# Performance work log

Measured on AMD Instinct MI355X. Metric: run time of the kernel, lower is better.

Reference implementation:

```python
import jax, jax.numpy as jnp
import numpy as np
from jax import lax

WINDOW_SIZE = 11
SIGMA = 1.5
DATA_RANGE = 1.0


def gaussian_window(size, sigma):
    k = jnp.arange(size, dtype=jnp.float32) - size // 2
    k = jnp.exp(-0.5 / sigma ** 2 * k ** 2)
    return k / k.sum()


def depthwise_conv(x, window):
    # x: [B,C,H,W], window: [C,1,k,k]
    pad = WINDOW_SIZE // 2
    return lax.conv_general_dilated(
        x, window,
        window_strides=(1, 1),
        padding=[(pad, pad), (pad, pad)],
        dimension_numbers=('NCHW', 'OIHW', 'NCHW'),
        feature_group_count=x.shape[1])


def setup_inputs() -> dict:
    key = jax.random.key(0)
    k1, k2 = jax.random.split(key)
    img1 = jax.random.uniform(k1, (32, 3, 512, 512), dtype=jnp.float32)
    img2 = jax.random.uniform(k2, (32, 3, 512, 512), dtype=jnp.float32)
    return {"img1": img1, "img2": img2}


def reference(img1, img2):
    channels = img1.shape[1]
    w1 = gaussian_window(WINDOW_SIZE, SIGMA)[:, None]        # [k,1]
    w2 = w1 @ w1.T                                           # [k,k]
    window = jnp.broadcast_to(w2, (channels, 1, WINDOW_SIZE, WINDOW_SIZE))

    C1 = (0.01 * DATA_RANGE) ** 2
    C2 = (0.03 * DATA_RANGE) ** 2

    mu1 = depthwise_conv(img1, window)
    mu2 = depthwise_conv(img2, window)
    mu1_sq = mu1 * mu1
    mu2_sq = mu2 * mu2
    mu1_mu2 = mu1 * mu2
    sigma1_sq = depthwise_conv(img1 * img1, window) - mu1_sq
    sigma2_sq = depthwise_conv(img2 * img2, window) - mu2_sq
    sigma12 = depthwise_conv(img1 * img2, window) - mu1_mu2

    ssim_map = ((2 * mu1_mu2 + C1) * (2 * sigma12 + C2)) / (
        (mu1_sq + mu2_sq + C1) * (sigma1_sq + sigma2_sq + C2))
    return 1.0 - ssim_map.mean()
```

## Files before the change

### kernel.cpp

```cpp
#include <hip/hip_runtime.h>
#include <math.h>

typedef float float2v __attribute__((ext_vector_type(2)));
typedef unsigned int u32;
typedef u32 u32x4 __attribute__((ext_vector_type(4)));
typedef _Float16 f16;
typedef f16 f16x2 __attribute__((ext_vector_type(2)));

#define NTHREADS 512

constexpr int H = 512, W = 512;
constexpr int TY = 16;
constexpr int NBANDS = H / TY;
constexpr int NPLANES = 96;
constexpr int NB = NBANDS * NPLANES;
constexpr int PITCH = 524;
constexpr int PAIR = 16 * PITCH;
constexpr double NTOT = 25165824.0;
constexpr float C1 = 1.0e-4f;
constexpr float C2 = 9.0e-4f;

struct Wts { float w[11]; };

__device__ __forceinline__ float2v up2(u32 w) {
    const f16x2 h = __builtin_bit_cast(f16x2, w);
    return (float2v){(float)h.x, (float)h.y};
}

template<bool EDGE>
__device__ __forceinline__ void do_column(const float* __restrict__ p1,
                                          const float* __restrict__ p2,
                                          u32* __restrict__ vc,
                                          const Wts& wts, int cc, int y0)
{
    const int x = cc - 5;
    const bool xok = (x >= 0) && (x < W);
    float2v ab[26], qq[26];
    #pragma unroll
    for (int t = 0; t < 26; ++t) {
        const int y = y0 - 5 + t;
        bool ok = xok;
        if (EDGE) ok = ok && (y >= 0) && (y < H);
        const float v1 = ok ? p1[y * W + x] : 0.f;
        const float v2 = ok ? p2[y * W + x] : 0.f;
        ab[t] = (float2v){v1 + v2, v1 - v2};
        qq[t] = ab[t] * ab[t];
    }
    u32* wp = vc + cc;
    #pragma unroll
    for (int r = 0; r < 16; ++r) {
        float2v sP = ab[r] * wts.w[0];
        float2v sQ = qq[r] * wts.w[0];
        #pragma unroll
        for (int k = 1; k < 11; ++k) {
            sP += ab[r + k] * wts.w[k];
            sQ += qq[r + k] * wts.w[k];
        }
        wp[r * PITCH]        = __builtin_bit_cast(u32, __builtin_amdgcn_cvt_pkrtz(sP.x, sP.y));
        wp[r * PITCH + PAIR] = __builtin_bit_cast(u32, __builtin_amdgcn_cvt_pkrtz(sQ.x, sQ.y));
    }
}

__global__ __launch_bounds__(NTHREADS, 4)
void ssim_main(const float* __restrict__ img1, const float* __restrict__ img2,
               float* __restrict__ part, Wts wts)
{
    __shared__ __align__(16) u32 vc[2 * 16 * PITCH];
    __shared__ float red[8];

    const int tid  = threadIdx.x;
    const int band = blockIdx.x;
    const int y0   = band * TY;
    const size_t plane = (size_t)blockIdx.y * (size_t)(H * W);
    const float* p1 = img1 + plane;
    const float* p2 = img2 + plane;

    if (band == 0 || band == NBANDS - 1) {
        do_column<true>(p1, p2, vc, wts, tid, y0);
        if (tid < 10) do_column<true>(p1, p2, vc, wts, 512 + tid, y0);
    } else {
        do_column<false>(p1, p2, vc, wts, tid, y0);
        if (tid < 10) do_column<false>(p1, p2, vc, wts, 512 + tid, y0);
    }
    __syncthreads();

    const int r = tid & 15;
    const int G = tid >> 4;
    const u32* row0 = vc + r * PITCH + 16 * G;

    float2v AB[26];
    #pragma unroll
    for (int i = 0; i < 7; ++i) {
        const u32x4 t4 = ((const u32x4*)row0)[i];
        #pragma unroll
        for (int e = 0; e < 4; ++e) {
            const int idx = 4 * i + e;
            if (idx < 26) AB[idx] = up2(t4[e]);
        }
    }
    float2v P[16];
    #pragma unroll
    for (int j = 0; j < 16; ++j) {
        float2v s = AB[j] * wts.w[0];
        #pragma unroll
        for (int k = 1; k < 11; ++k) s += AB[j + k] * wts.w[k];
        P[j] = s;
    }

    const u32* row1 = row0 + PAIR;
    float2v QQ[26];
    #pragma unroll
    for (int i = 0; i < 7; ++i) {
        const u32x4 t4 = ((const u32x4*)row1)[i];
        #pragma unroll
        for (int e = 0; e < 4; ++e) {
            const int idx = 4 * i + e;
            if (idx < 26) QQ[idx] = up2(t4[e]);
        }
    }

    float local = 0.f;
    #pragma unroll
    for (int j = 0; j < 16; ++j) {
        float2v sq = QQ[j] * wts.w[0];
        #pragma unroll
        for (int k = 1; k < 11; ++k) sq += QQ[j + k] * wts.w[k];
        const float A  = P[j].x, B = P[j].y;
        const float Qa = sq.x,  Qb = sq.y;
        const float u = A * A, v = B * B;
        const float t1 = u - v;
        const float t2 = u + v;
        const float num1 = fmaf(0.5f, t1, C1);
        const float den1 = fmaf(0.5f, t2, C1);
        const float num2 = fmaf(0.5f, (Qa - Qb) - t1, C2);
        const float den2 = fmaf(0.5f, (Qa + Qb) - t2, C2);
        local += (num1 * num2) * __builtin_amdgcn_rcpf(den1 * den2);
    }

    #pragma unroll
    for (int off = 32; off > 0; off >>= 1) local += __shfl_down(local, off, 64);
    if ((tid & 63) == 0) red[tid >> 6] = local;
    __syncthreads();
    if (tid == 0) {
        float s = 0.f;
        #pragma unroll
        for (int wv = 0; wv < 8; ++wv) s += red[wv];
        part[blockIdx.y * NBANDS + band] = s;
    }
}

__global__ __launch_bounds__(512)
void ssim_final(const float* __restrict__ part, float* __restrict__ out)
{
    __shared__ double red[8];
    const int tid = threadIdx.x;
    double s = 0.0;
    for (int i = tid; i < NB; i += 512) s += (double)part[i];
    #pragma unroll
    for (int off = 32; off > 0; off >>= 1) s += __shfl_down(s, off, 64);
    if ((tid & 63) == 0) red[tid >> 6] = s;
    __syncthreads();
    if (tid == 0) {
        double t = 0.0;
        #pragma unroll
        for (int wv = 0; wv < 8; ++wv) t += red[wv];
        out[0] = (float)(1.0 - t / NTOT);
    }
}

extern "C" void kernel_launch(void* const* d_in, const int* in_sizes, int n_in,
                              void* d_out, int out_size, void* d_ws, size_t ws_size,
                              hipStream_t stream)
{
    const float* img1 = (const float*)d_in[0];
    const float* img2 = (const float*)d_in[1];
    float* out = (float*)d_out;
    float* part = (float*)d_ws;

    Wts wts;
    double wd[11], s = 0.0;
    for (int k = 0; k < 11; ++k) {
        const double d = (double)(k - 5);
        wd[k] = exp(-0.5 / (1.5 * 1.5) * d * d);
        s += wd[k];
    }
    for (int k = 0; k < 11; ++k) wts.w[k] = (float)(wd[k] / s);

    dim3 grid(NBANDS, NPLANES);
    ssim_main<<<grid, NTHREADS, 0, stream>>>(img1, img2, part, wts);
    ssim_final<<<1, 512, 0, stream>>>(part, out);
}
```

Measured before the change: 242.5 us.

## Compute separable Gaussian blurs as banded-matrix MFMA products in fp16

Replaces the scalar vertical and horizontal 11-tap convolutions with MFMA 16x16x32 fp16 matrix multiplies against a banded Toeplitz weight matrix built in shared memory. Each wave processes 16-column tiles, loading 8 rows per lane group, converting sums, differences and their squares to fp16 and running four MFMAs per pass. This is meant to offload the FMA-heavy convolution work to the matrix cores. The risk is extra precision loss, because the inputs and squares are now rounded to fp16 before the vertical pass as well, and global loads become strided per lane.

```diff
diff --git a/kernel.cpp b/kernel.cpp
--- a/kernel.cpp
+++ b/kernel.cpp
@@ -1,145 +1,128 @@
 #include <hip/hip_runtime.h>
 #include <math.h>
 
-typedef float float2v __attribute__((ext_vector_type(2)));
+typedef _Float16 f16;
+typedef f16 f16x8 __attribute__((ext_vector_type(8)));
+typedef f16 f16x2 __attribute__((ext_vector_type(2)));
+typedef float f32x4 __attribute__((ext_vector_type(4)));
 typedef unsigned int u32;
-typedef u32 u32x4 __attribute__((ext_vector_type(4)));
-typedef _Float16 f16;
-typedef f16 f16x2 __attribute__((ext_vector_type(2)));
-
-#define NTHREADS 512
+typedef u32 u32x2 __attribute__((ext_vector_type(2)));
 
 constexpr int H = 512, W = 512;
 constexpr int TY = 16;
 constexpr int NBANDS = H / TY;
 constexpr int NPLANES = 96;
 constexpr int NB = NBANDS * NPLANES;
-constexpr int PITCH = 524;
-constexpr int PAIR = 16 * PITCH;
+constexpr int VP = 552;
 constexpr double NTOT = 25165824.0;
 constexpr float C1 = 1.0e-4f;
 constexpr float C2 = 9.0e-4f;
 
 struct Wts { float w[11]; };
 
-__device__ __forceinline__ float2v up2(u32 w) {
-    const f16x2 h = __builtin_bit_cast(f16x2, w);
-    return (float2v){(float)h.x, (float)h.y};
+__device__ __forceinline__ u32 pk(float lo, float hi) {
+    return __builtin_bit_cast(u32, __builtin_amdgcn_cvt_pkrtz(lo, hi));
 }
 
-template<bool EDGE>
-__device__ __forceinline__ void do_column(const float* __restrict__ p1,
-                                          const float* __restrict__ p2,
-                                          u32* __restrict__ vc,
-                                          const Wts& wts, int cc, int y0)
-{
-    const int x = cc - 5;
-    const bool xok = (x >= 0) && (x < W);
-    float2v ab[26], qq[26];
-    #pragma unroll
-    for (int t = 0; t < 26; ++t) {
-        const int y = y0 - 5 + t;
-        bool ok = xok;
-        if (EDGE) ok = ok && (y >= 0) && (y < H);
-        const float v1 = ok ? p1[y * W + x] : 0.f;
-        const float v2 = ok ? p2[y * W + x] : 0.f;
-        ab[t] = (float2v){v1 + v2, v1 - v2};
-        qq[t] = ab[t] * ab[t];
-    }
-    u32* wp = vc + cc;
-    #pragma unroll
-    for (int r = 0; r < 16; ++r) {
-        float2v sP = ab[r] * wts.w[0];
-        float2v sQ = qq[r] * wts.w[0];
-        #pragma unroll
-        for (int k = 1; k < 11; ++k) {
-            sP += ab[r + k] * wts.w[k];
-            sQ += qq[r + k] * wts.w[k];
-        }
-        wp[r * PITCH]        = __builtin_bit_cast(u32, __builtin_amdgcn_cvt_pkrtz(sP.x, sP.y));
-        wp[r * PITCH + PAIR] = __builtin_bit_cast(u32, __builtin_amdgcn_cvt_pkrtz(sQ.x, sQ.y));
-    }
-}
-
-__global__ __launch_bounds__(NTHREADS, 4)
+__global__ __launch_bounds__(512, 4)
 void ssim_main(const float* __restrict__ img1, const float* __restrict__ img2,
                float* __restrict__ part, Wts wts)
 {
-    __shared__ __align__(16) u32 vc[2 * 16 * PITCH];
+    __shared__ __align__(16) f16 vc[4][TY][VP];
+    __shared__ __align__(16) f16 Tb[16][40];
     __shared__ float red[8];
 
     const int tid  = threadIdx.x;
+    const int lane = tid & 63;
+    const int wave = tid >> 6;
+    const int tr   = lane & 15;
+    const int g    = lane >> 4;
+    const int k0   = g * 8;
+
+    for (int i = tid; i < 640; i += 512) {
+        const int m = i / 40, k = i - m * 40, d = k - m;
+        Tb[m][k] = (d >= 0 && d <= 10) ? (f16)wts.w[d] : (f16)0.0f;
+    }
+    __syncthreads();
+    const f16x8 tw = *(const f16x8*)&Tb[tr][k0];
+
     const int band = blockIdx.x;
     const int y0   = band * TY;
     const size_t plane = (size_t)blockIdx.y * (size_t)(H * W);
     const float* p1 = img1 + plane;
     const float* p2 = img2 + plane;
 
-    if (band == 0 || band == NBANDS - 1) {
-        do_column<true>(p1, p2, vc, wts, tid, y0);
-        if (tid < 10) do_column<true>(p1, p2, vc, wts, 512 + tid, y0);
-    } else {
-        do_column<false>(p1, p2, vc, wts, tid, y0);
-        if (tid < 10) do_column<false>(p1, p2, vc, wts, 512 + tid, y0);
+    int   rowbase[8];
+    float ymul[8];
+    #pragma unroll
+    for (int j = 0; j < 8; ++j) {
+        const int y = y0 - 5 + k0 + j;
+        const bool yok = (unsigned)y < (unsigned)H;
+        rowbase[j] = (yok ? y : 0) * W;
+        ymul[j] = yok ? 1.f : 0.f;
+    }
+
+    const f32x4 z4 = { 0.f, 0.f, 0.f, 0.f };
+
+    for (int t = wave; t < 33; t += 8) {
+        const int x   = 16 * t + tr - 5;
+        const bool xok = (unsigned)x < (unsigned)W;
+        const int xc  = xok ? x : 0;
+        const float xm = xok ? 1.f : 0.f;
+
+        f16x8 fA, fB, fQa, fQb;
+        #pragma unroll
+        for (int j = 0; j < 8; ++j) {
+            const float m  = xm * ymul[j];
+            const float a1 = p1[rowbase[j] + xc] * m;
+            const float a2 = p2[rowbase[j] + xc] * m;
+            const float a = a1 + a2, b = a1 - a2;
+            fA[j]  = (f16)a;        fB[j]  = (f16)b;
+            fQa[j] = (f16)(a * a);  fQb[j] = (f16)(b * b);
+        }
+        const f32x4 dA  = __builtin_amdgcn_mfma_f32_16x16x32_f16(fA,  tw, z4, 0, 0, 0);
+        const f32x4 dB  = __builtin_amdgcn_mfma_f32_16x16x32_f16(fB,  tw, z4, 0, 0, 0);
+        const f32x4 dQa = __builtin_amdgcn_mfma_f32_16x16x32_f16(fQa, tw, z4, 0, 0, 0);
+        const f32x4 dQb = __builtin_amdgcn_mfma_f32_16x16x32_f16(fQb, tw, z4, 0, 0, 0);
+
+        const int cb = 16 * t + 4 * g;
+        { u32x2 v = { pk(dA[0],  dA[1]),  pk(dA[2],  dA[3])  }; *(u32x2*)&vc[0][tr][cb] = v; }
+        { u32x2 v = { pk(dB[0],  dB[1]),  pk(dB[2],  dB[3])  }; *(u32x2*)&vc[1][tr][cb] = v; }
+        { u32x2 v = { pk(dQa[0], dQa[1]), pk(dQa[2], dQa[3]) }; *(u32x2*)&vc[2][tr][cb] = v; }
+        { u32x2 v = { pk(dQb[0], dQb[1]), pk(dQb[2], dQb[3]) }; *(u32x2*)&vc[3][tr][cb] = v; }
     }
     __syncthreads();
 
-    const int r = tid & 15;
-    const int G = tid >> 4;
-    const u32* row0 = vc + r * PITCH + 16 * G;
+    float local = 0.f;
+    for (int t = wave; t < 32; t += 8) {
+        const int cb = 16 * t;
+        const f16x8 bA  = *(const f16x8*)&vc[0][tr][cb + k0];
+        const f16x8 bB  = *(const f16x8*)&vc[1][tr][cb + k0];
+        const f16x8 bQa = *(const f16x8*)&vc[2][tr][cb + k0];
+        const f16x8 bQb = *(const f16x8*)&vc[3][tr][cb + k0];
+        const f32x4 rA  = __builtin_amdgcn_mfma_f32_16x16x32_f16(tw, bA,  z4, 0, 0, 0);
+        const f32x4 rB  = __builtin_amdgcn_mfma_f32_16x16x32_f16(tw, bB,  z4, 0, 0, 0);
+        const f32x4 rQa = __builtin_amdgcn_mfma_f32_16x16x32_f16(tw, bQa, z4, 0, 0, 0);
+        const f32x4 rQb = __builtin_amdgcn_mfma_f32_16x16x32_f16(tw, bQb, z4, 0, 0, 0);
 
-    float2v AB[26];
-    #pragma unroll
-    for (int i = 0; i < 7; ++i) {
-        const u32x4 t4 = ((const u32x4*)row0)[i];
         #pragma unroll
-        for (int e = 0; e < 4; ++e) {
-            const int idx = 4 * i + e;
-            if (idx < 26) AB[idx] = up2(t4[e]);
+        for (int i = 0; i < 4; ++i) {
+            const float A  = rA[i],  Bv = rB[i];
+            const float Qa = rQa[i], Qb = rQb[i];
+            const float u = A * A, v = Bv * Bv;
+            const float t1 = u - v;
+            const float t2 = u + v;
+            const float num1 = fmaf(0.5f, t1, C1);
+            const float den1 = fmaf(0.5f, t2, C1);
+            const float num2 = fmaf(0.5f, (Qa - Qb) - t1, C2);
+            const float den2 = fmaf(0.5f, (Qa + Qb) - t2, C2);
+            local += (num1 * num2) * __builtin_amdgcn_rcpf(den1 * den2);
         }
-    }
-    float2v P[16];
-    #pragma unroll
-    for (int j = 0; j < 16; ++j) {
-        float2v s = AB[j] * wts.w[0];
-        #pragma unroll
-        for (int k = 1; k < 11; ++k) s += AB[j + k] * wts.w[k];
-        P[j] = s;
-    }
-
-    const u32* row1 = row0 + PAIR;
-    float2v QQ[26];
-    #pragma unroll
-    for (int i = 0; i < 7; ++i) {
-        const u32x4 t4 = ((const u32x4*)row1)[i];
-        #pragma unroll
-        for (int e = 0; e < 4; ++e) {
-            const int idx = 4 * i + e;
-            if (idx < 26) QQ[idx] = up2(t4[e]);
-        }
-    }
-
-    float local = 0.f;
-    #pragma unroll
-    for (int j = 0; j < 16; ++j) {
-        float2v sq = QQ[j] * wts.w[0];
-        #pragma unroll
-        for (int k = 1; k < 11; ++k) sq += QQ[j + k] * wts.w[k];
-        const float A  = P[j].x, B = P[j].y;
-        const float Qa = sq.x,  Qb = sq.y;
-        const float u = A * A, v = B * B;
-        const float t1 = u - v;
-        const float t2 = u + v;
-        const float num1 = fmaf(0.5f, t1, C1);
-        const float den1 = fmaf(0.5f, t2, C1);
-        const float num2 = fmaf(0.5f, (Qa - Qb) - t1, C2);
-        const float den2 = fmaf(0.5f, (Qa + Qb) - t2, C2);
-        local += (num1 * num2) * __builtin_amdgcn_rcpf(den1 * den2);
     }
 
     #pragma unroll
     for (int off = 32; off > 0; off >>= 1) local += __shfl_down(local, off, 64);
-    if ((tid & 63) == 0) red[tid >> 6] = local;
+    if (lane == 0) red[wave] = local;
     __syncthreads();
     if (tid == 0) {
         float s = 0.f;
@@ -187,6 +170,6 @@
     for (int k = 0; k < 11; ++k) wts.w[k] = (float)(wd[k] / s);
 
     dim3 grid(NBANDS, NPLANES);
-    ssim_main<<<grid, NTHREADS, 0, stream>>>(img1, img2, part, wts);
+    ssim_main<<<grid, 512, 0, stream>>>(img1, img2, part, wts);
     ssim_final<<<1, 512, 0, stream>>>(part, out);
 }
```

Result: faster. 227.1 us (-6.3%).
